# Performance work log

Hardware: AMD Instinct MI355X
Metric: run time of the kernel (lower is better)

The kernel has to match this reference:

```python
import jax, jax.numpy as jnp
import numpy as np

B, V = 256, 128000

def setup_inputs() -> dict:
    key = jax.random.key(0)
    k1, k2, k3, k4, k5 = jax.random.split(key, 5)
    logits = jax.random.normal(k1, (B, V), jnp.float32) * 4.0
    temperatures = jax.random.uniform(k2, (B, 1), jnp.float32, 0.5, 1.5)
    top_ps = jax.random.uniform(k3, (B, 1), jnp.float32, 0.5, 1.0)
    top_ks = jax.random.randint(k4, (B, 1), 1, 64).astype(jnp.float32)
    # uniform noise for Gumbel-max sampling (replaces torch's internal RNG)
    noise = jax.random.uniform(k5, (B, V), jnp.float32, 1e-6, 1.0 - 1e-6)
    return {"logits": logits, "temperatures": temperatures, "top_ps": top_ps,
            "top_ks": top_ks, "noise": noise}

def reference(logits, temperatures, top_ps, top_ks, noise):
    # temperature scale (torch: logits.div_(temperatures)); guard temp==0 rows
    safe_t = jnp.where(temperatures == 0.0, 1.0, temperatures)
    scaled = logits / safe_t  # [B, V]; this is the returned `probs` in the torch path
    probs = jax.nn.softmax(scaled, axis=-1)
    # sort probs descending over vocab
    order = jnp.argsort(-probs, axis=-1)                 # [B, V] original token ids
    sp = jnp.take_along_axis(probs, order, axis=-1)      # sorted probs desc
    cdf_excl = jnp.cumsum(sp, axis=-1) - sp              # exclusive cumsum
    ranks = jnp.arange(V, dtype=jnp.float32)[None, :]
    # joint top-k AND top-p mask (flashinfer 'joint' filter_apply_order)
    keep = (ranks < top_ks) & (cdf_excl <= top_ps)       # rank 0 always kept
    logp = jnp.where(keep, jnp.log(jnp.where(keep, sp, 1.0)), -jnp.inf)
    # Gumbel-max sample among kept tokens (renormalization-invariant)
    gumbel = -jnp.log(-jnp.log(noise))
    idx_sorted = jnp.argmax(logp + gumbel, axis=-1)      # [B]
    token = jnp.take_along_axis(order, idx_sorted[:, None], axis=-1)[:, 0]
    # temperature == 0 rows fall back to greedy argmax of original logits
    greedy = jnp.argmax(logits, axis=-1)
    token = jnp.where(temperatures[:, 0] == 0.0, greedy, token)
    return token.astype(jnp.int32), scaled
```

## Files before the change

### kernel.cpp

```cpp
#include <hip/hip_runtime.h>
#include <math.h>

#define VOCAB   128000
#define VOCAB4  32000
#define NROW    256
#define TOPC    63
#define HPR     2
#define BS      1024
#define H4      (VOCAB4 / HPR)
#define TAILT   (H4 - 15 * BS)
#define LCAP    320
#define CAP     512
#define T0      11.0f
#define BSM     512

typedef float f32x4 __attribute__((ext_vector_type(4)));


__device__ __forceinline__ unsigned ordf(float v) {
  unsigned u = __float_as_uint(v);
  return (u & 0x80000000u) ? ~u : (u | 0x80000000u);
}

__device__ __forceinline__ void proc4(
    float4 x, int j4, float inv_t, float4* __restrict__ o4,
    float& s0, float& s1, float& s2, float& s3,
    unsigned int* nc, float* cv, int* ci)
{
  float vx = x.x*inv_t, vy = x.y*inv_t, vz = x.z*inv_t, vw = x.w*inv_t;
  f32x4 v = {vx, vy, vz, vw};
  *(f32x4*)&o4[j4] = v;
  s0 += __expf(vx); s1 += __expf(vy); s2 += __expf(vz); s3 += __expf(vw);
  if (x.x > T0) { unsigned q = atomicAdd(nc,1u); if (q<LCAP){cv[q]=vx; ci[q]=4*j4+0;} }
  if (x.y > T0) { unsigned q = atomicAdd(nc,1u); if (q<LCAP){cv[q]=vy; ci[q]=4*j4+1;} }
  if (x.z > T0) { unsigned q = atomicAdd(nc,1u); if (q<LCAP){cv[q]=vz; ci[q]=4*j4+2;} }
  if (x.w > T0) { unsigned q = atomicAdd(nc,1u); if (q<LCAP){cv[q]=vw; ci[q]=4*j4+3;} }
}

__global__ __launch_bounds__(BS, 8) void stream_kernel(
    const float* __restrict__ logits, const float* __restrict__ temps,
    float* __restrict__ out, unsigned int* __restrict__ cnt,
    float* __restrict__ psum, float* __restrict__ cval, int* __restrict__ cidx)
{
  const int blk = blockIdx.x;
  const int row = blk >> 1;
  const int hh  = blk & 1;
  const int tid = threadIdx.x;

  __shared__ float lcv[LCAP]; __shared__ int lci[LCAP];
  __shared__ float wsum[BS / 64];
  __shared__ unsigned int nc_sh, base_sh;

  if (tid == 0) nc_sh = 0u;
  __syncthreads();

  const float temp  = temps[row];
  const float inv_t = 1.0f / ((temp == 0.0f) ? 1.0f : temp);

  const float4* __restrict__ lg4 =
      reinterpret_cast<const float4*>(logits + (size_t)row * VOCAB);
  float4* __restrict__ o4 =
      reinterpret_cast<float4*>(out + NROW + (size_t)row * VOCAB);

  float s0 = 0.f, s1 = 0.f, s2 = 0.f, s3 = 0.f;

  int j = hh * H4 + tid;
  #pragma unroll
  for (int g = 0; g < 7; ++g) {
    float4 a = lg4[j];
    float4 b = lg4[j + BS];
    proc4(a, j,      inv_t, o4, s0,s1,s2,s3, &nc_sh, lcv, lci);
    proc4(b, j + BS, inv_t, o4, s0,s1,s2,s3, &nc_sh, lcv, lci);
    j += 2 * BS;
  }
  {
    float4 a = lg4[j];
    proc4(a, j, inv_t, o4, s0,s1,s2,s3, &nc_sh, lcv, lci);
  }
  if (tid < TAILT) {
    int jt = hh * H4 + 15 * BS + tid;
    float4 a = lg4[jt];
    proc4(a, jt, inv_t, o4, s0,s1,s2,s3, &nc_sh, lcv, lci);
  }

  float s = (s0 + s1) + (s2 + s3);
  #pragma unroll
  for (int off = 32; off > 0; off >>= 1) s += __shfl_down(s, off);
  if ((tid & 63) == 0) wsum[tid >> 6] = s;
  __syncthreads();
  if (tid == 0) {
    float t = 0.f;
    #pragma unroll
    for (int w = 0; w < BS / 64; ++w) t += wsum[w];
    psum[row * HPR + hh] = t;
    base_sh = atomicAdd(&cnt[row], (nc_sh < (unsigned)LCAP) ? nc_sh : (unsigned)LCAP);
  }
  __syncthreads();

  const int nloc = ((int)nc_sh < LCAP) ? (int)nc_sh : LCAP;
  const unsigned base = base_sh;
  for (int i = tid; i < nloc; i += BS) {
    unsigned p = base + i;
    if (p < CAP) { cval[row * CAP + p] = lcv[i]; cidx[row * CAP + p] = lci[i]; }
  }
}

__global__ __launch_bounds__(BSM) void merge_kernel(
    const float* __restrict__ logits, const float* __restrict__ temps,
    const float* __restrict__ topps, const float* __restrict__ topks,
    const float* __restrict__ noise, float* __restrict__ out,
    const unsigned int* __restrict__ cnt, const float* __restrict__ psum,
    const float* __restrict__ cval, const int* __restrict__ cidx)
{
  const int row = blockIdx.x;
  const int tid = threadIdx.x;

  __shared__ float cv2[CAP]; __shared__ int ci2[CAP];
  __shared__ unsigned long long kv[CAP];
  __shared__ float sv[64];   __shared__ int si[64];
  __shared__ float sp_s[64], sc_s[64], noi_s[64];
  __shared__ unsigned int nc2;

  if (tid < 64) noi_s[tid] = noise[(size_t)row * VOCAB + tid];

  const float temp  = temps[row];
  const float inv_t = 1.0f / ((temp == 0.0f) ? 1.0f : temp);
  const float S = psum[row * HPR + 0] + psum[row * HPR + 1];

  int total = (int)cnt[row];
  int n = (total < CAP) ? total : CAP;
  for (int i = tid; i < n; i += BSM) {
    cv2[i] = cval[row * CAP + i];
    ci2[i] = cidx[row * CAP + i];
  }
  __syncthreads();

  float thr = T0;
  for (int att = 0; att < 4 && (total < TOPC || total > CAP); ++att) {
    thr = (total > CAP) ? (thr + 2.0f) : (thr - 4.0f);
    __syncthreads();
    if (tid == 0) nc2 = 0u;
    __syncthreads();
    const float* __restrict__ lg = logits + (size_t)row * VOCAB;
    for (int k = tid; k < VOCAB; k += BSM) {
      float x = lg[k];
      if (x > thr) {
        unsigned p = atomicAdd(&nc2, 1u);
        if (p < CAP) { cv2[p] = x * inv_t; ci2[p] = k; }
      }
    }
    __syncthreads();
    total = (int)nc2;
    n = (total < CAP) ? total : CAP;
  }

  if (tid < n)
    kv[tid] = ((unsigned long long)(~ordf(cv2[tid])) << 32) | (unsigned)ci2[tid];
  __syncthreads();

  if (tid < n) {
    const unsigned long long me = kv[tid];
    int r = 0;
    #pragma unroll 8
    for (int k = 0; k < n; ++k) r += (int)(kv[k] < me);
    if (r < 64) { sv[r] = cv2[tid]; si[r] = ci2[tid]; }
  }
  __syncthreads();

  const int lim = (n < TOPC) ? n : TOPC;

  if (tid < lim) {
    float sp = __expf(sv[tid]) * (1.0f / S);
    sp_s[tid] = sp;
    float u = noi_s[tid];
    sc_s[tid] = logf(sp) + (-logf(-logf(u)));
  }
  __syncthreads();

  if (tid == 0) {
    const float kk = topks[row];
    const float tp = topps[row];
    float cdf = 0.f, best = -INFINITY; int bestj = 0;
    for (int k = 0; k < lim; ++k) {
      if (((float)k < kk) && (cdf <= tp)) {
        float sc = sc_s[k];
        if (sc > best) { best = sc; bestj = k; }
      }
      cdf += sp_s[k];
    }
    int token = (n > 0) ? si[bestj] : 0;
    if (temp == 0.0f && n > 0) token = si[0];
    out[row] = (float)token;
  }
}

extern "C" void kernel_launch(void* const* d_in, const int* in_sizes, int n_in,
                              void* d_out, int out_size, void* d_ws, size_t ws_size,
                              hipStream_t stream) {
  const float* logits = (const float*)d_in[0];
  const float* temps  = (const float*)d_in[1];
  const float* topps  = (const float*)d_in[2];
  const float* topks  = (const float*)d_in[3];
  const float* noise  = (const float*)d_in[4];
  float* out = (float*)d_out;

  char* ws = (char*)d_ws;
  unsigned int* cnt = (unsigned int*)(ws);
  float* psum = (float*)(ws + 1024);
  float* cval = (float*)(ws + 4096);
  int*   cidx = (int*)  (ws + 4096 + (size_t)NROW * CAP * 4);

  hipMemsetAsync(cnt, 0, 1024, stream);
  stream_kernel<<<NROW * HPR, BS, 0, stream>>>(logits, temps, out, cnt, psum, cval, cidx);
  merge_kernel<<<NROW, BSM, 0, stream>>>(logits, temps, topps, topks, noise, out,
                                         cnt, psum, cval, cidx);
}
```

Measured before the change: 77.24 us.

## Split each row across four smaller blocks and drop the global counter memset

The streaming kernel now splits each vocabulary row into four quarters handled by 512-thread blocks instead of two halves handled by 1024-thread blocks. Each block writes its candidates to a fixed per-quarter slot with its own count, so the global atomic counter and the memset launch are no longer needed. The merge kernel compacts the four candidate segments into shared memory and loops over more than 512 candidates in its rank sort. This adds more, smaller blocks for better load balance and removes one launch, at the cost of a slightly larger candidate buffer and a little more merge work.

```diff
diff --git a/kernel.cpp b/kernel.cpp
--- a/kernel.cpp
+++ b/kernel.cpp
@@ -5,12 +5,13 @@
 #define VOCAB4  32000
 #define NROW    256
 #define TOPC    63
-#define HPR     2
-#define BS      1024
-#define H4      (VOCAB4 / HPR)
-#define TAILT   (H4 - 15 * BS)
-#define LCAP    320
-#define CAP     512
+#define HPR     4
+#define BS      512
+#define Q4      (VOCAB4 / HPR)
+#define FIT     15
+#define TAILT   (Q4 - FIT * BS)
+#define LCAP    192
+#define CAPR    (HPR * LCAP)
 #define T0      11.0f
 #define BSM     512
 
@@ -39,17 +40,17 @@
 
 __global__ __launch_bounds__(BS, 8) void stream_kernel(
     const float* __restrict__ logits, const float* __restrict__ temps,
-    float* __restrict__ out, unsigned int* __restrict__ cnt,
+    float* __restrict__ out, unsigned int* __restrict__ cnt4,
     float* __restrict__ psum, float* __restrict__ cval, int* __restrict__ cidx)
 {
   const int blk = blockIdx.x;
-  const int row = blk >> 1;
-  const int hh  = blk & 1;
+  const int row = blk >> 2;
+  const int qq  = blk & 3;
   const int tid = threadIdx.x;
 
   __shared__ float lcv[LCAP]; __shared__ int lci[LCAP];
   __shared__ float wsum[BS / 64];
-  __shared__ unsigned int nc_sh, base_sh;
+  __shared__ unsigned int nc_sh;
 
   if (tid == 0) nc_sh = 0u;
   __syncthreads();
@@ -64,7 +65,7 @@
 
   float s0 = 0.f, s1 = 0.f, s2 = 0.f, s3 = 0.f;
 
-  int j = hh * H4 + tid;
+  int j = qq * Q4 + tid;
   #pragma unroll
   for (int g = 0; g < 7; ++g) {
     float4 a = lg4[j];
@@ -78,7 +79,7 @@
     proc4(a, j, inv_t, o4, s0,s1,s2,s3, &nc_sh, lcv, lci);
   }
   if (tid < TAILT) {
-    int jt = hh * H4 + 15 * BS + tid;
+    int jt = qq * Q4 + FIT * BS + tid;
     float4 a = lg4[jt];
     proc4(a, jt, inv_t, o4, s0,s1,s2,s3, &nc_sh, lcv, lci);
   }
@@ -92,16 +93,15 @@
     float t = 0.f;
     #pragma unroll
     for (int w = 0; w < BS / 64; ++w) t += wsum[w];
-    psum[row * HPR + hh] = t;
-    base_sh = atomicAdd(&cnt[row], (nc_sh < (unsigned)LCAP) ? nc_sh : (unsigned)LCAP);
+    psum[row * HPR + qq] = t;
+    cnt4[row * HPR + qq] = nc_sh;
   }
   __syncthreads();
 
   const int nloc = ((int)nc_sh < LCAP) ? (int)nc_sh : LCAP;
-  const unsigned base = base_sh;
   for (int i = tid; i < nloc; i += BS) {
-    unsigned p = base + i;
-    if (p < CAP) { cval[row * CAP + p] = lcv[i]; cidx[row * CAP + p] = lci[i]; }
+    cval[row * CAPR + qq * LCAP + i] = lcv[i];
+    cidx[row * CAPR + qq * LCAP + i] = lci[i];
   }
 }
 
@@ -109,14 +109,14 @@
     const float* __restrict__ logits, const float* __restrict__ temps,
     const float* __restrict__ topps, const float* __restrict__ topks,
     const float* __restrict__ noise, float* __restrict__ out,
-    const unsigned int* __restrict__ cnt, const float* __restrict__ psum,
+    const unsigned int* __restrict__ cnt4, const float* __restrict__ psum,
     const float* __restrict__ cval, const int* __restrict__ cidx)
 {
   const int row = blockIdx.x;
   const int tid = threadIdx.x;
 
-  __shared__ float cv2[CAP]; __shared__ int ci2[CAP];
-  __shared__ unsigned long long kv[CAP];
+  __shared__ float cv2[CAPR]; __shared__ int ci2[CAPR];
+  __shared__ unsigned long long kv[CAPR];
   __shared__ float sv[64];   __shared__ int si[64];
   __shared__ float sp_s[64], sc_s[64], noi_s[64];
   __shared__ unsigned int nc2;
@@ -125,19 +125,33 @@
 
   const float temp  = temps[row];
   const float inv_t = 1.0f / ((temp == 0.0f) ? 1.0f : temp);
-  const float S = psum[row * HPR + 0] + psum[row * HPR + 1];
-
-  int total = (int)cnt[row];
-  int n = (total < CAP) ? total : CAP;
-  for (int i = tid; i < n; i += BSM) {
-    cv2[i] = cval[row * CAP + i];
-    ci2[i] = cidx[row * CAP + i];
-  }
+  const float S = (psum[row*HPR+0] + psum[row*HPR+1]) +
+                  (psum[row*HPR+2] + psum[row*HPR+3]);
+
+  unsigned raw0 = cnt4[row*HPR+0], raw1 = cnt4[row*HPR+1];
+  unsigned raw2 = cnt4[row*HPR+2], raw3 = cnt4[row*HPR+3];
+  int c0 = (raw0 < LCAP) ? (int)raw0 : LCAP;
+  int c1 = (raw1 < LCAP) ? (int)raw1 : LCAP;
+  int c2 = (raw2 < LCAP) ? (int)raw2 : LCAP;
+  int c3 = (raw3 < LCAP) ? (int)raw3 : LCAP;
+  bool ovf = (raw0 > LCAP) | (raw1 > LCAP) | (raw2 > LCAP) | (raw3 > LCAP);
+  int off1 = c0, off2 = c0 + c1, off3 = c0 + c1 + c2;
+  int total = ovf ? (CAPR + 1) : (c0 + c1 + c2 + c3);
+  int n = (total < CAPR) ? total : CAPR;
+
+  for (int i = tid; i < c0; i += BSM) {
+    cv2[i] = cval[row*CAPR + 0*LCAP + i]; ci2[i] = cidx[row*CAPR + 0*LCAP + i]; }
+  for (int i = tid; i < c1; i += BSM) {
+    cv2[off1+i] = cval[row*CAPR + 1*LCAP + i]; ci2[off1+i] = cidx[row*CAPR + 1*LCAP + i]; }
+  for (int i = tid; i < c2; i += BSM) {
+    cv2[off2+i] = cval[row*CAPR + 2*LCAP + i]; ci2[off2+i] = cidx[row*CAPR + 2*LCAP + i]; }
+  for (int i = tid; i < c3; i += BSM) {
+    cv2[off3+i] = cval[row*CAPR + 3*LCAP + i]; ci2[off3+i] = cidx[row*CAPR + 3*LCAP + i]; }
   __syncthreads();
 
   float thr = T0;
-  for (int att = 0; att < 4 && (total < TOPC || total > CAP); ++att) {
-    thr = (total > CAP) ? (thr + 2.0f) : (thr - 4.0f);
+  for (int att = 0; att < 4 && (total < TOPC || total > CAPR); ++att) {
+    thr = (total > CAPR) ? (thr + 2.0f) : (thr - 4.0f);
     __syncthreads();
     if (tid == 0) nc2 = 0u;
     __syncthreads();
@@ -146,24 +160,24 @@
       float x = lg[k];
       if (x > thr) {
         unsigned p = atomicAdd(&nc2, 1u);
-        if (p < CAP) { cv2[p] = x * inv_t; ci2[p] = k; }
+        if (p < CAPR) { cv2[p] = x * inv_t; ci2[p] = k; }
       }
     }
     __syncthreads();
     total = (int)nc2;
-    n = (total < CAP) ? total : CAP;
-  }
-
-  if (tid < n)
-    kv[tid] = ((unsigned long long)(~ordf(cv2[tid])) << 32) | (unsigned)ci2[tid];
-  __syncthreads();
-
-  if (tid < n) {
-    const unsigned long long me = kv[tid];
+    n = (total < CAPR) ? total : CAPR;
+  }
+
+  for (int i = tid; i < n; i += BSM)
+    kv[i] = ((unsigned long long)(~ordf(cv2[i])) << 32) | (unsigned)ci2[i];
+  __syncthreads();
+
+  for (int i = tid; i < n; i += BSM) {
+    const unsigned long long me = kv[i];
     int r = 0;
     #pragma unroll 8
     for (int k = 0; k < n; ++k) r += (int)(kv[k] < me);
-    if (r < 64) { sv[r] = cv2[tid]; si[r] = ci2[tid]; }
+    if (r < 64) { sv[r] = cv2[i]; si[r] = ci2[i]; }
   }
   __syncthreads();
 
@@ -205,13 +219,12 @@
   float* out = (float*)d_out;
 
   char* ws = (char*)d_ws;
-  unsigned int* cnt = (unsigned int*)(ws);
-  float* psum = (float*)(ws + 1024);
-  float* cval = (float*)(ws + 4096);
-  int*   cidx = (int*)  (ws + 4096 + (size_t)NROW * CAP * 4);
-
-  hipMemsetAsync(cnt, 0, 1024, stream);
-  stream_kernel<<<NROW * HPR, BS, 0, stream>>>(logits, temps, out, cnt, psum, cval, cidx);
+  unsigned int* cnt4 = (unsigned int*)(ws);
+  float* psum = (float*)(ws + 4096);
+  float* cval = (float*)(ws + 8192);
+  int*   cidx = (int*)  (ws + 8192 + (size_t)NROW * CAPR * 4);
+
+  stream_kernel<<<NROW * HPR, BS, 0, stream>>>(logits, temps, out, cnt4, psum, cval, cidx);
   merge_kernel<<<NROW, BSM, 0, stream>>>(logits, temps, topps, topks, noise, out,
-                                         cnt, psum, cval, cidx);
-}
+                                         cnt4, psum, cval, cidx);
+}
```

Measured after the change: 74.15 us. 4.0% less time.
